# Optimization experiments

Measured on AMD Instinct MI355X. Metric: run time of the kernel, lower is better.

## Reference

```python
import jax, jax.numpy as jnp
import numpy as np

NEG_SLOPE = 0.2
N_NODES = 50000


def gat_conv(x, src, dst, W, a_src, a_dst, b, n_nodes):
    """One PyG-style GATConv layer (eval mode, self-loops already in src/dst).
    x: [N, F_in]; W: [F_in, H*C]; a_src/a_dst: [H, C]; b: [H*C] or [C].
    Returns per-node, per-head outputs [N, H, C].
    """
    H, C = a_src.shape
    h = (x @ W).reshape(-1, H, C)                      # [N, H, C]
    s_src = jnp.sum(h * a_src[None], axis=-1)          # [N, H]
    s_dst = jnp.sum(h * a_dst[None], axis=-1)          # [N, H]
    e = jax.nn.leaky_relu(s_src[src] + s_dst[dst], NEG_SLOPE)   # [E, H]
    # segment softmax over incoming edges of each destination node
    m = jax.ops.segment_max(e, dst, num_segments=n_nodes)       # [N, H]
    w = jnp.exp(e - m[dst])                                     # [E, H]
    denom = jax.ops.segment_sum(w, dst, num_segments=n_nodes)   # [N, H]
    alpha = w / denom[dst]                                      # [E, H]
    # weighted aggregation of source features
    out = jax.ops.segment_sum(alpha[:, :, None] * h[src], dst, num_segments=n_nodes)
    return out  # [N, H, C]


def setup_inputs() -> dict:
    key = jax.random.key(0)
    ks = jax.random.split(key, 12)
    N, F_in, Hid, H, F_out = N_NODES, 128, 64, 4, 128
    E = 800000
    x = jax.random.normal(ks[0], (N, F_in), dtype=jnp.float32)
    edge_index = jax.random.randint(ks[1], (2, E), 0, N, dtype=jnp.int64)
    sc = 0.1
    return {
        "x": x,
        "edge_index": edge_index,
        "W1": jax.random.normal(ks[2], (F_in, H * Hid), dtype=jnp.float32) * sc,
        "att_src1": jax.random.normal(ks[3], (H, Hid), dtype=jnp.float32) * sc,
        "att_dst1": jax.random.normal(ks[4], (H, Hid), dtype=jnp.float32) * sc,
        "b1": jnp.zeros((H * Hid,), dtype=jnp.float32),
        "W2": jax.random.normal(ks[5], (H * Hid, F_out), dtype=jnp.float32) * sc,
        "att_src2": jax.random.normal(ks[6], (1, F_out), dtype=jnp.float32) * sc,
        "att_dst2": jax.random.normal(ks[7], (1, F_out), dtype=jnp.float32) * sc,
        "b2": jnp.zeros((F_out,), dtype=jnp.float32),
    }


def reference(x, edge_index, W1, att_src1, att_dst1, b1, W2, att_src2, att_dst2, b2):
    N = x.shape[0]
    # PyG GATConv adds self-loops by default
    loops = jnp.arange(N, dtype=edge_index.dtype)
    src = jnp.concatenate([edge_index[0], loops])
    dst = jnp.concatenate([edge_index[1], loops])
    # layer 1: heads=4, concat -> [N, H*Hid], then ELU (dropout is identity in eval)
    h1 = gat_conv(x, src, dst, W1, att_src1, att_dst1, b1, N)    # [N, H, Hid]
    h1 = h1.reshape(N, -1) + b1
    h1 = jax.nn.elu(h1)
    # layer 2: heads=1, concat=False -> mean over the single head
    h2 = gat_conv(h1, src, dst, W2, att_src2, att_dst2, b2, N)   # [N, 1, F_out]
    out = h2[:, 0, :] + b2
    return out
```

## Files before the change

kernel.cpp:

```cpp
#include <hip/hip_runtime.h>
#include <cmath>

typedef __attribute__((ext_vector_type(8))) short bf16x8;
typedef __attribute__((ext_vector_type(4))) float f32x4;

static __device__ __forceinline__ unsigned short f2bf(float f) {
    unsigned u = __float_as_uint(f);
    unsigned r = (u + 0x7fffu + ((u >> 16) & 1u)) >> 16;
    return (unsigned short)r;
}
static __device__ __forceinline__ unsigned packbf(float a, float b) {
    return (unsigned)f2bf(a) | ((unsigned)f2bf(b) << 16);
}
static __device__ __forceinline__ float bflo(unsigned u) { return __uint_as_float(u << 16); }
static __device__ __forceinline__ float bfhi(unsigned u) { return __uint_as_float(u & 0xffff0000u); }

__global__ void prep_k(const float* __restrict__ x, const float* __restrict__ W1,
                       const float* __restrict__ W2, const int* __restrict__ dst,
                       unsigned* __restrict__ xb,
                       unsigned short* __restrict__ Wt1, unsigned short* __restrict__ Wt2,
                       int* __restrict__ deg, int NX2, int NW1, int NW2, int E) {
    int i = blockIdx.x * blockDim.x + threadIdx.x;
    if (i < NX2) {
        float2 v = reinterpret_cast<const float2*>(x)[i];
        xb[i] = packbf(v.x, v.y);
        return;
    }
    i -= NX2;
    if (i < NW1) { int nn = i / 128, k = i % 128; Wt1[i] = f2bf(W1[(size_t)k * 256 + nn]); return; }
    i -= NW1;
    if (i < NW2) { int nn = i / 256, k = i % 256; Wt2[i] = f2bf(W2[(size_t)k * 128 + nn]); return; }
    i -= NW2;
    if (i < E) atomicAdd(&deg[dst[i]], 1);
}

#define SCAN_BLK 256
#define SCAN_ELEMS 2048

__global__ void scan1_k(const int* __restrict__ deg, int* __restrict__ rowstart,
                        int* __restrict__ bsums, int N) {
    __shared__ int sh[SCAN_BLK];
    int t = threadIdx.x;
    int base = blockIdx.x * SCAN_ELEMS + t * 8;
    int vals[8];
    int sum = 0;
#pragma unroll
    for (int i = 0; i < 8; ++i) {
        int idx = base + i;
        vals[i] = (idx < N) ? (deg[idx] + 1) : 0;
        sum += vals[i];
    }
    sh[t] = sum;
    __syncthreads();
    for (int off = 1; off < SCAN_BLK; off <<= 1) {
        int v = (t >= off) ? sh[t - off] : 0;
        __syncthreads();
        sh[t] += v;
        __syncthreads();
    }
    int run = sh[t] - sum;
    if (t == SCAN_BLK - 1) bsums[blockIdx.x] = sh[t];
#pragma unroll
    for (int i = 0; i < 8; ++i) {
        int idx = base + i;
        if (idx < N) rowstart[idx] = run;
        run += vals[i];
    }
}
__global__ void scan2_k(int* __restrict__ bsums, int nb) {
    int lane = threadIdx.x;
    int own = (lane < nb) ? bsums[lane] : 0;
    int v = own;
    for (int off = 1; off < 64; off <<= 1) {
        int t = __shfl_up(v, off, 64);
        if (lane >= off) v += t;
    }
    if (lane < nb) bsums[lane] = v - own;
}
__global__ void scan3_init_k(int* __restrict__ rowstart, const int* __restrict__ bsums,
                             int* __restrict__ adj, int* __restrict__ cursor, int N, int total) {
    int i = blockIdx.x * blockDim.x + threadIdx.x;
    if (i < N) {
        int r = rowstart[i] + bsums[i / SCAN_ELEMS];
        rowstart[i] = r;
        adj[r] = i;
        cursor[i] = r + 1;
    } else if (i == N) {
        rowstart[N] = total;
    }
}
__global__ void scatter_k(const int* __restrict__ src, const int* __restrict__ dst, int E,
                          int* __restrict__ cursor, int* __restrict__ adj) {
    int e = blockIdx.x * blockDim.x + threadIdx.x;
    if (e >= E) return;
    int pos = atomicAdd(&cursor[dst[e]], 1);
    adj[pos] = src[e];
}

template<int K, int NOUT, int H, int C>
__global__ __launch_bounds__(256) void gemm_score_k(const unsigned* __restrict__ Ab,
                                                    const unsigned* __restrict__ Bt,
                                                    unsigned short* __restrict__ Yb,
                                                    const float* __restrict__ asrc,
                                                    const float* __restrict__ adst,
                                                    float* __restrict__ ssrc,
                                                    float* __restrict__ sdst, int N) {
    __shared__ unsigned short As[128 * 64];
    __shared__ unsigned short Bs[64 * 64];
    __shared__ float sred[2][2][128];
    int tid = threadIdx.x;
    int lane = tid & 63, wid = tid >> 6;
    int wm = wid >> 1, wc = wid & 1;
    int m0 = blockIdx.x * 128;
    int n0 = blockIdx.y * 64;

    f32x4 acc[4][2] = {};

    for (int k0 = 0; k0 < K; k0 += 64) {
#pragma unroll
        for (int p = 0; p < 4; ++p) {
            int gl = p * 256 + tid;
            int row = gl >> 3, g = gl & 7;
            int grow = m0 + row; if (grow >= N) grow = N - 1;
            uint4 v = *reinterpret_cast<const uint4*>(Ab + (size_t)grow * (K / 2) + k0 / 2 + g * 4);
            *reinterpret_cast<uint4*>((char*)As + row * 128 + ((g ^ (row & 7)) << 4)) = v;
        }
#pragma unroll
        for (int p = 0; p < 2; ++p) {
            int gl = p * 256 + tid;
            int row = gl >> 3, g = gl & 7;
            uint4 v = *reinterpret_cast<const uint4*>(Bt + (size_t)(n0 + row) * (K / 2) + k0 / 2 + g * 4);
            *reinterpret_cast<uint4*>((char*)Bs + row * 128 + ((g ^ (row & 7)) << 4)) = v;
        }
        __syncthreads();

        bf16x8 bfrag[2][2];
#pragma unroll
        for (int kk = 0; kk < 2; ++kk)
#pragma unroll
            for (int no = 0; no < 2; ++no) {
                int row = wc * 32 + no * 16 + (lane & 15);
                int g = kk * 4 + (lane >> 4);
                bfrag[kk][no] = *reinterpret_cast<const bf16x8*>((char*)Bs + row * 128 + ((g ^ (row & 7)) << 4));
            }
#pragma unroll
        for (int mo = 0; mo < 4; ++mo) {
#pragma unroll
            for (int kk = 0; kk < 2; ++kk) {
                int row = wm * 64 + mo * 16 + (lane & 15);
                int g = kk * 4 + (lane >> 4);
                bf16x8 afrag = *reinterpret_cast<const bf16x8*>((char*)As + row * 128 + ((g ^ (row & 7)) << 4));
                acc[mo][0] = __builtin_amdgcn_mfma_f32_16x16x32_bf16(afrag, bfrag[kk][0], acc[mo][0], 0, 0, 0);
                acc[mo][1] = __builtin_amdgcn_mfma_f32_16x16x32_bf16(afrag, bfrag[kk][1], acc[mo][1], 0, 0, 0);
            }
        }
        __syncthreads();
    }

#pragma unroll
    for (int mo = 0; mo < 4; ++mo)
#pragma unroll
        for (int no = 0; no < 2; ++no) {
            int col = n0 + wc * 32 + no * 16 + (lane & 15);
            int rbase = m0 + wm * 64 + mo * 16 + (lane >> 4) * 4;
#pragma unroll
            for (int j = 0; j < 4; ++j) {
                int row = rbase + j;
                if (row < N) Yb[(size_t)row * NOUT + col] = f2bf(acc[mo][no][j]);
            }
        }

    float cs0, cs1, cd0, cd1;
    {
        int c0 = n0 + wc * 32 + (lane & 15);
        cs0 = asrc[c0]; cd0 = adst[c0];
        cs1 = asrc[c0 + 16]; cd1 = adst[c0 + 16];
    }
#pragma unroll
    for (int mo = 0; mo < 4; ++mo) {
        float ps[4], pd[4];
#pragma unroll
        for (int j = 0; j < 4; ++j) {
            ps[j] = acc[mo][0][j] * cs0 + acc[mo][1][j] * cs1;
            pd[j] = acc[mo][0][j] * cd0 + acc[mo][1][j] * cd1;
        }
#pragma unroll
        for (int off = 8; off; off >>= 1)
#pragma unroll
            for (int j = 0; j < 4; ++j) {
                ps[j] += __shfl_xor(ps[j], off, 64);
                pd[j] += __shfl_xor(pd[j], off, 64);
            }
        if ((lane & 15) == 0) {
            int rl = wm * 64 + mo * 16 + (lane >> 4) * 4;
#pragma unroll
            for (int j = 0; j < 4; ++j) {
                sred[wc][0][rl + j] = ps[j];
                sred[wc][1][rl + j] = pd[j];
            }
        }
    }
    __syncthreads();
    if (tid < 128) {
        int grow = m0 + tid;
        if (grow < N) {
            float fs = sred[0][0][tid] + sred[1][0][tid];
            float fd = sred[0][1][tid] + sred[1][1][tid];
            if constexpr (C <= 64) {
                int hh = n0 / C;
                ssrc[(size_t)grow * H + hh] = fs;
                sdst[(size_t)grow * H + hh] = fd;
            } else {
                atomicAdd(&ssrc[grow], fs);
                atomicAdd(&sdst[grow], fd);
            }
        }
    }
}

template<int H, int C, int GRP, bool ELU, bool OUT_BF16>
__global__ void node_agg_k(const int* __restrict__ rowstart, const int* __restrict__ adj,
                           const float* __restrict__ ssrc, const float* __restrict__ sdst,
                           const unsigned* __restrict__ hb, const float* __restrict__ bias,
                           void* __restrict__ outp, int N) {
    constexpr int HC = H * C;
    constexpr int ROW_U = HC / 2;
    constexpr int ULN = ROW_U / GRP;
    constexpr int FPLn = ULN * 2;
    constexpr int NG = 64 / GRP;
    constexpr int NGB = 4 * NG;
    int lane = threadIdx.x & 63;
    int w = threadIdx.x >> 6;
    int g = lane / GRP, ln = lane % GRP;
    int gid = w * NG + g;
    int n = blockIdx.x * NGB + gid;
    if (n >= N) return;

    __shared__ int   s_tab[NGB][64];
    __shared__ float a_tab[NGB][64 * H];

    int r0 = rowstart[n], r1 = rowstart[n + 1];
    int deg = r1 - r0;

    float sd[H];
#pragma unroll
    for (int h = 0; h < H; ++h) sd[h] = sdst[n * H + h];

    int hA = (ln * FPLn) / C;
    const unsigned* hbl = hb + ln * ULN;
    float acc[FPLn];
#pragma unroll
    for (int f = 0; f < FPLn; ++f) acc[f] = 0.f;
    float l[H];
#pragma unroll
    for (int h = 0; h < H; ++h) l[h] = 0.f;

    if (deg <= 64) {
        for (int base = 0; base < deg; base += GRP) {
            int idx = base + ln;
            bool on = idx < deg;
            int s = adj[r0 + (on ? idx : 0)];
            float v[H];
            if constexpr (H == 4) {
                float4 sv = reinterpret_cast<const float4*>(ssrc)[s];
                v[0] = sv.x; v[1] = sv.y; v[2] = sv.z; v[3] = sv.w;
            } else {
                v[0] = ssrc[s];
            }
#pragma unroll
            for (int h = 0; h < H; ++h) {
                float t = v[h] + sd[h];
                t = t > 0.f ? t : 0.2f * t;
                float av = on ? __expf(t) : 0.f;
                l[h] += av;
                if (on) a_tab[gid][idx * H + h] = av;
            }
            if (on) s_tab[gid][idx] = s;
        }
#pragma unroll
        for (int off = GRP / 2; off; off >>= 1)
#pragma unroll
            for (int h = 0; h < H; ++h) l[h] += __shfl_xor(l[h], off, 64);

        int j = 0;
        for (; j + 3 < deg; j += 4) {
            int s0 = s_tab[gid][j],     s1 = s_tab[gid][j + 1];
            int s2 = s_tab[gid][j + 2], s3 = s_tab[gid][j + 3];
            float a0 = a_tab[gid][j * H + hA],       a1 = a_tab[gid][(j + 1) * H + hA];
            float a2 = a_tab[gid][(j + 2) * H + hA], a3 = a_tab[gid][(j + 3) * H + hA];
            uint4 u0 = *reinterpret_cast<const uint4*>(hbl + (size_t)s0 * ROW_U);
            uint4 u1 = *reinterpret_cast<const uint4*>(hbl + (size_t)s1 * ROW_U);
            uint4 u2 = *reinterpret_cast<const uint4*>(hbl + (size_t)s2 * ROW_U);
            uint4 u3 = *reinterpret_cast<const uint4*>(hbl + (size_t)s3 * ROW_U);
            acc[0] += a0 * bflo(u0.x); acc[1] += a0 * bfhi(u0.x);
            acc[2] += a0 * bflo(u0.y); acc[3] += a0 * bfhi(u0.y);
            acc[4] += a0 * bflo(u0.z); acc[5] += a0 * bfhi(u0.z);
            acc[6] += a0 * bflo(u0.w); acc[7] += a0 * bfhi(u0.w);
            acc[0] += a1 * bflo(u1.x); acc[1] += a1 * bfhi(u1.x);
            acc[2] += a1 * bflo(u1.y); acc[3] += a1 * bfhi(u1.y);
            acc[4] += a1 * bflo(u1.z); acc[5] += a1 * bfhi(u1.z);
            acc[6] += a1 * bflo(u1.w); acc[7] += a1 * bfhi(u1.w);
            acc[0] += a2 * bflo(u2.x); acc[1] += a2 * bfhi(u2.x);
            acc[2] += a2 * bflo(u2.y); acc[3] += a2 * bfhi(u2.y);
            acc[4] += a2 * bflo(u2.z); acc[5] += a2 * bfhi(u2.z);
            acc[6] += a2 * bflo(u2.w); acc[7] += a2 * bfhi(u2.w);
            acc[0] += a3 * bflo(u3.x); acc[1] += a3 * bfhi(u3.x);
            acc[2] += a3 * bflo(u3.y); acc[3] += a3 * bfhi(u3.y);
            acc[4] += a3 * bflo(u3.z); acc[5] += a3 * bfhi(u3.z);
            acc[6] += a3 * bflo(u3.w); acc[7] += a3 * bfhi(u3.w);
        }
        for (; j < deg; ++j) {
            int sj = s_tab[gid][j];
            float al = a_tab[gid][j * H + hA];
            uint4 u = *reinterpret_cast<const uint4*>(hbl + (size_t)sj * ROW_U);
            acc[0] += al * bflo(u.x); acc[1] += al * bfhi(u.x);
            acc[2] += al * bflo(u.y); acc[3] += al * bfhi(u.y);
            acc[4] += al * bflo(u.z); acc[5] += al * bfhi(u.z);
            acc[6] += al * bflo(u.w); acc[7] += al * bfhi(u.w);
        }
    } else {
        for (int e = r0 + ln; e < r1; e += GRP) {
            int s = adj[e];
#pragma unroll
            for (int h = 0; h < H; ++h) {
                float t = ssrc[s * H + h] + sd[h];
                t = t > 0.f ? t : 0.2f * t;
                l[h] += __expf(t);
            }
        }
#pragma unroll
        for (int off = GRP / 2; off; off >>= 1)
#pragma unroll
            for (int h = 0; h < H; ++h) l[h] += __shfl_xor(l[h], off, 64);
        float sdh = sd[hA];
        for (int e = r0; e < r1; ++e) {
            int s = adj[e];
            float t = ssrc[s * H + hA] + sdh;
            t = t > 0.f ? t : 0.2f * t;
            float al = __expf(t);
            uint4 u = *reinterpret_cast<const uint4*>(hbl + (size_t)s * ROW_U);
            acc[0] += al * bflo(u.x); acc[1] += al * bfhi(u.x);
            acc[2] += al * bflo(u.y); acc[3] += al * bfhi(u.y);
            acc[4] += al * bflo(u.z); acc[5] += al * bfhi(u.z);
            acc[6] += al * bflo(u.w); acc[7] += al * bfhi(u.w);
        }
    }

    float invl = __builtin_amdgcn_rcpf(l[hA]);
#pragma unroll
    for (int f = 0; f < FPLn; ++f) {
        float v = acc[f] * invl + bias[ln * FPLn + f];
        if (ELU) v = v > 0.f ? v : (__expf(v) - 1.f);
        acc[f] = v;
    }
    if constexpr (OUT_BF16) {
        unsigned* op = (unsigned*)outp + (size_t)n * ROW_U + ln * ULN;
        uint4 u = {packbf(acc[0], acc[1]), packbf(acc[2], acc[3]),
                   packbf(acc[4], acc[5]), packbf(acc[6], acc[7])};
        *reinterpret_cast<uint4*>(op) = u;
    } else {
        float* op = (float*)outp + (size_t)n * HC + ln * FPLn;
        *reinterpret_cast<float4*>(op) = make_float4(acc[0], acc[1], acc[2], acc[3]);
        *reinterpret_cast<float4*>(op + 4) = make_float4(acc[4], acc[5], acc[6], acc[7]);
    }
}

extern "C" void kernel_launch(void* const* d_in, const int* in_sizes, int n_in,
                              void* d_out, int out_size, void* d_ws, size_t ws_size,
                              hipStream_t stream) {
    const float* x   = (const float*)d_in[0];
    const int*   ei  = (const int*)d_in[1];
    const float* W1  = (const float*)d_in[2];
    const float* as1 = (const float*)d_in[3];
    const float* ad1 = (const float*)d_in[4];
    const float* b1  = (const float*)d_in[5];
    const float* W2  = (const float*)d_in[6];
    const float* as2 = (const float*)d_in[7];
    const float* ad2 = (const float*)d_in[8];
    const float* b2  = (const float*)d_in[9];
    float* out = (float*)d_out;

    const int N  = in_sizes[0] / 128;
    const int E  = in_sizes[1] / 2;
    const int ET = E + N;
    const int* src = ei;
    const int* dst = ei + E;

    unsigned* ws = (unsigned*)d_ws;
    unsigned* xb    = ws;
    unsigned* h1b   = xb    + (size_t)N * 64;
    unsigned* agg1b = h1b   + (size_t)N * 128;
    unsigned* h2b   = agg1b + (size_t)N * 128;
    unsigned* Wt1   = h2b   + (size_t)N * 64;
    unsigned* Wt2   = Wt1   + 16384;
    float*    ssrc1 = (float*)(Wt2 + 16384);
    float*    sdst1 = ssrc1 + (size_t)N * 4;
    float*    ssrc2 = sdst1 + (size_t)N * 4;
    float*    sdst2 = ssrc2 + N;
    int*      deg   = (int*)(sdst2 + N);
    int*      rowst = deg + N;
    int*      bsums = rowst + N + 1;
    int*      adj   = bsums + 64;

    const int B = 256;
    auto blocks = [](size_t n, int b) { return (int)((n + b - 1) / b); };
    const int nscan = (N + SCAN_ELEMS - 1) / SCAN_ELEMS;

    hipMemsetAsync(ssrc2, 0, (size_t)N * 3 * 4, stream);
    {
        int NX2 = N * 64, NW1 = 128 * 256, NW2 = 256 * 128;
        size_t tot = (size_t)NX2 + NW1 + NW2 + E;
        prep_k<<<blocks(tot, B), B, 0, stream>>>(x, W1, W2, dst, xb, (unsigned short*)Wt1,
                                                 (unsigned short*)Wt2, deg, NX2, NW1, NW2, E);
    }

    scan1_k<<<nscan, SCAN_BLK, 0, stream>>>(deg, rowst, bsums, N);
    scan2_k<<<1, 64, 0, stream>>>(bsums, nscan);
    scan3_init_k<<<blocks(N + 1, B), B, 0, stream>>>(rowst, bsums, adj, deg, N, ET);
    scatter_k<<<blocks(E, B), B, 0, stream>>>(src, dst, E, deg, adj);

    {
        dim3 g((N + 127) / 128, 256 / 64);
        gemm_score_k<128, 256, 4, 64><<<g, 256, 0, stream>>>(
            xb, (const unsigned*)Wt1, (unsigned short*)h1b, as1, ad1, ssrc1, sdst1, N);
    }
    node_agg_k<4, 64, 32, true, true><<<(N + 7) / 8, 256, 0, stream>>>(rowst, adj, ssrc1, sdst1, h1b, b1, agg1b, N);

    {
        dim3 g((N + 127) / 128, 128 / 64);
        gemm_score_k<256, 128, 1, 128><<<g, 256, 0, stream>>>(
            agg1b, (const unsigned*)Wt2, (unsigned short*)h2b, as2, ad2, ssrc2, sdst2, N);
    }
    node_agg_k<1, 128, 16, false, false><<<(N + 15) / 16, 256, 0, stream>>>(rowst, adj, ssrc2, sdst2, h2b, b2, out, N);
}
```

Measured before the change: 244.8 us.

## Fuse CSR scan into single chained-scan kernel and widen aggregation unroll

Replaces the three-kernel scan (block scan, block-sum scan, finalize) with one kernel that uses a decoupled chained prefix via atomic flags, so each block spin-waits on its predecessor. The chain flags are zeroed inside the existing prep kernel. This removes two kernel launches and their serialization gaps. The node aggregation also transposes the attention table to a head-major layout and unrolls the gather loop to 8 independent loads for more memory-level parallelism. The spin-wait assumes earlier blocks are scheduled first, which holds for the small grid here (about 25 blocks).

```diff
diff --git a/kernel.cpp b/kernel.cpp
--- a/kernel.cpp
+++ b/kernel.cpp
@@ -15,11 +15,15 @@
 static __device__ __forceinline__ float bflo(unsigned u) { return __uint_as_float(u << 16); }
 static __device__ __forceinline__ float bfhi(unsigned u) { return __uint_as_float(u & 0xffff0000u); }
 
+#define SCAN_BLK 256
+#define SCAN_ELEMS 2048
+
 __global__ void prep_k(const float* __restrict__ x, const float* __restrict__ W1,
                        const float* __restrict__ W2, const int* __restrict__ dst,
                        unsigned* __restrict__ xb,
                        unsigned short* __restrict__ Wt1, unsigned short* __restrict__ Wt2,
-                       int* __restrict__ deg, int NX2, int NW1, int NW2, int E) {
+                       int* __restrict__ deg, int* __restrict__ chain,
+                       int NX2, int NW1, int NW2, int E, int NCH) {
     int i = blockIdx.x * blockDim.x + threadIdx.x;
     if (i < NX2) {
         float2 v = reinterpret_cast<const float2*>(x)[i];
@@ -31,17 +35,18 @@
     i -= NW1;
     if (i < NW2) { int nn = i / 256, k = i % 256; Wt2[i] = f2bf(W2[(size_t)k * 128 + nn]); return; }
     i -= NW2;
-    if (i < E) atomicAdd(&deg[dst[i]], 1);
-}
-
-#define SCAN_BLK 256
-#define SCAN_ELEMS 2048
-
-__global__ void scan1_k(const int* __restrict__ deg, int* __restrict__ rowstart,
-                        int* __restrict__ bsums, int N) {
+    if (i < E) { atomicAdd(&deg[dst[i]], 1); return; }
+    i -= E;
+    if (i < NCH) chain[i] = 0;
+}
+
+__global__ void csr_build_k(const int* __restrict__ deg, int* __restrict__ rowstart,
+                            int* __restrict__ adj, int* __restrict__ cursor,
+                            int* __restrict__ chain, int N, int total) {
     __shared__ int sh[SCAN_BLK];
-    int t = threadIdx.x;
-    int base = blockIdx.x * SCAN_ELEMS + t * 8;
+    __shared__ int s_prefix;
+    int t = threadIdx.x, b = blockIdx.x;
+    int base = b * SCAN_ELEMS + t * 8;
     int vals[8];
     int sum = 0;
 #pragma unroll
@@ -59,36 +64,32 @@
         __syncthreads();
     }
     int run = sh[t] - sum;
-    if (t == SCAN_BLK - 1) bsums[blockIdx.x] = sh[t];
+    int blocksum = sh[SCAN_BLK - 1];
+    if (t == 0) {
+        int prev = 0;
+        if (b > 0) {
+            int c;
+            while ((c = __hip_atomic_load(&chain[b], __ATOMIC_ACQUIRE, __HIP_MEMORY_SCOPE_AGENT)) == 0) {}
+            prev = c - 1;
+        }
+        __hip_atomic_store(&chain[b + 1], prev + blocksum + 1, __ATOMIC_RELEASE, __HIP_MEMORY_SCOPE_AGENT);
+        s_prefix = prev;
+    }
+    __syncthreads();
+    int r = run + s_prefix;
 #pragma unroll
     for (int i = 0; i < 8; ++i) {
         int idx = base + i;
-        if (idx < N) rowstart[idx] = run;
-        run += vals[i];
-    }
-}
-__global__ void scan2_k(int* __restrict__ bsums, int nb) {
-    int lane = threadIdx.x;
-    int own = (lane < nb) ? bsums[lane] : 0;
-    int v = own;
-    for (int off = 1; off < 64; off <<= 1) {
-        int t = __shfl_up(v, off, 64);
-        if (lane >= off) v += t;
-    }
-    if (lane < nb) bsums[lane] = v - own;
-}
-__global__ void scan3_init_k(int* __restrict__ rowstart, const int* __restrict__ bsums,
-                             int* __restrict__ adj, int* __restrict__ cursor, int N, int total) {
-    int i = blockIdx.x * blockDim.x + threadIdx.x;
-    if (i < N) {
-        int r = rowstart[i] + bsums[i / SCAN_ELEMS];
-        rowstart[i] = r;
-        adj[r] = i;
-        cursor[i] = r + 1;
-    } else if (i == N) {
-        rowstart[N] = total;
-    }
-}
+        if (idx < N) {
+            rowstart[idx] = r;
+            adj[r] = idx;
+            cursor[idx] = r + 1;
+        }
+        r += vals[i];
+    }
+    if (b == gridDim.x - 1 && t == SCAN_BLK - 1) rowstart[N] = total;
+}
+
 __global__ void scatter_k(const int* __restrict__ src, const int* __restrict__ dst, int E,
                           int* __restrict__ cursor, int* __restrict__ adj) {
     int e = blockIdx.x * blockDim.x + threadIdx.x;
@@ -237,7 +238,7 @@
     if (n >= N) return;
 
     __shared__ int   s_tab[NGB][64];
-    __shared__ float a_tab[NGB][64 * H];
+    __shared__ float a_tab[NGB][H][64];
 
     int r0 = rowstart[n], r1 = rowstart[n + 1];
     int deg = r1 - r0;
@@ -273,7 +274,7 @@
                 t = t > 0.f ? t : 0.2f * t;
                 float av = on ? __expf(t) : 0.f;
                 l[h] += av;
-                if (on) a_tab[gid][idx * H + h] = av;
+                if (on) a_tab[gid][h][idx] = av;
             }
             if (on) s_tab[gid][idx] = s;
         }
@@ -282,16 +283,27 @@
 #pragma unroll
             for (int h = 0; h < H; ++h) l[h] += __shfl_xor(l[h], off, 64);
 
+        const float* atab = a_tab[gid][hA];
         int j = 0;
-        for (; j + 3 < deg; j += 4) {
-            int s0 = s_tab[gid][j],     s1 = s_tab[gid][j + 1];
-            int s2 = s_tab[gid][j + 2], s3 = s_tab[gid][j + 3];
-            float a0 = a_tab[gid][j * H + hA],       a1 = a_tab[gid][(j + 1) * H + hA];
-            float a2 = a_tab[gid][(j + 2) * H + hA], a3 = a_tab[gid][(j + 3) * H + hA];
+        for (; j + 7 < deg; j += 8) {
+            int ss[8]; float aa[8]; uint4 uu[8];
+#pragma unroll
+            for (int q = 0; q < 8; ++q) { ss[q] = s_tab[gid][j + q]; aa[q] = atab[j + q]; }
+#pragma unroll
+            for (int q = 0; q < 8; ++q) uu[q] = *reinterpret_cast<const uint4*>(hbl + (size_t)ss[q] * ROW_U);
+#pragma unroll
+            for (int q = 0; q < 8; ++q) {
+                acc[0] += aa[q] * bflo(uu[q].x); acc[1] += aa[q] * bfhi(uu[q].x);
+                acc[2] += aa[q] * bflo(uu[q].y); acc[3] += aa[q] * bfhi(uu[q].y);
+                acc[4] += aa[q] * bflo(uu[q].z); acc[5] += aa[q] * bfhi(uu[q].z);
+                acc[6] += aa[q] * bflo(uu[q].w); acc[7] += aa[q] * bfhi(uu[q].w);
+            }
+        }
+        for (; j + 1 < deg; j += 2) {
+            int s0 = s_tab[gid][j], s1 = s_tab[gid][j + 1];
+            float a0 = atab[j], a1 = atab[j + 1];
             uint4 u0 = *reinterpret_cast<const uint4*>(hbl + (size_t)s0 * ROW_U);
             uint4 u1 = *reinterpret_cast<const uint4*>(hbl + (size_t)s1 * ROW_U);
-            uint4 u2 = *reinterpret_cast<const uint4*>(hbl + (size_t)s2 * ROW_U);
-            uint4 u3 = *reinterpret_cast<const uint4*>(hbl + (size_t)s3 * ROW_U);
             acc[0] += a0 * bflo(u0.x); acc[1] += a0 * bfhi(u0.x);
             acc[2] += a0 * bflo(u0.y); acc[3] += a0 * bfhi(u0.y);
             acc[4] += a0 * bflo(u0.z); acc[5] += a0 * bfhi(u0.z);
@@ -300,18 +312,10 @@
             acc[2] += a1 * bflo(u1.y); acc[3] += a1 * bfhi(u1.y);
             acc[4] += a1 * bflo(u1.z); acc[5] += a1 * bfhi(u1.z);
             acc[6] += a1 * bflo(u1.w); acc[7] += a1 * bfhi(u1.w);
-            acc[0] += a2 * bflo(u2.x); acc[1] += a2 * bfhi(u2.x);
-            acc[2] += a2 * bflo(u2.y); acc[3] += a2 * bfhi(u2.y);
-            acc[4] += a2 * bflo(u2.z); acc[5] += a2 * bfhi(u2.z);
-            acc[6] += a2 * bflo(u2.w); acc[7] += a2 * bfhi(u2.w);
-            acc[0] += a3 * bflo(u3.x); acc[1] += a3 * bfhi(u3.x);
-            acc[2] += a3 * bflo(u3.y); acc[3] += a3 * bfhi(u3.y);
-            acc[4] += a3 * bflo(u3.z); acc[5] += a3 * bfhi(u3.z);
-            acc[6] += a3 * bflo(u3.w); acc[7] += a3 * bfhi(u3.w);
-        }
-        for (; j < deg; ++j) {
+        }
+        if (j < deg) {
             int sj = s_tab[gid][j];
-            float al = a_tab[gid][j * H + hA];
+            float al = atab[j];
             uint4 u = *reinterpret_cast<const uint4*>(hbl + (size_t)sj * ROW_U);
             acc[0] += al * bflo(u.x); acc[1] += al * bfhi(u.x);
             acc[2] += al * bflo(u.y); acc[3] += al * bfhi(u.y);
@@ -399,8 +403,8 @@
     float*    sdst2 = ssrc2 + N;
     int*      deg   = (int*)(sdst2 + N);
     int*      rowst = deg + N;
-    int*      bsums = rowst + N + 1;
-    int*      adj   = bsums + 64;
+    int*      chain = rowst + N + 1;
+    int*      adj   = chain + 128;
 
     const int B = 256;
     auto blocks = [](size_t n, int b) { return (int)((n + b - 1) / b); };
@@ -409,14 +413,13 @@
     hipMemsetAsync(ssrc2, 0, (size_t)N * 3 * 4, stream);
     {
         int NX2 = N * 64, NW1 = 128 * 256, NW2 = 256 * 128;
-        size_t tot = (size_t)NX2 + NW1 + NW2 + E;
+        size_t tot = (size_t)NX2 + NW1 + NW2 + E + (nscan + 1);
         prep_k<<<blocks(tot, B), B, 0, stream>>>(x, W1, W2, dst, xb, (unsigned short*)Wt1,
-                                                 (unsigned short*)Wt2, deg, NX2, NW1, NW2, E);
-    }
-
-    scan1_k<<<nscan, SCAN_BLK, 0, stream>>>(deg, rowst, bsums, N);
-    scan2_k<<<1, 64, 0, stream>>>(bsums, nscan);
-    scan3_init_k<<<blocks(N + 1, B), B, 0, stream>>>(rowst, bsums, adj, deg, N, ET);
+                                                 (unsigned short*)Wt2, deg, chain,
+                                                 NX2, NW1, NW2, E, nscan + 1);
+    }
+
+    csr_build_k<<<nscan, SCAN_BLK, 0, stream>>>(deg, rowst, adj, deg, chain, N, ET);
     scatter_k<<<blocks(E, B), B, 0, stream>>>(src, dst, E, deg, adj);
 
     {
```

After: 265.2 us. 1.08x slower.
